# Optimization experiments

Hardware: AMD Instinct MI355X
Metric: run time of the kernel (lower is better)

## Reference

```python
import jax, jax.numpy as jnp
import numpy as np
from jax import lax


def _conv(x, w):
    # x: [B,H,W,C], w: [kh,kw,Cin,Cout], stride 1, 'same' padding
    return lax.conv_general_dilated(x, w, window_strides=(1, 1), padding='SAME',
                                    dimension_numbers=('NHWC', 'HWIO', 'NHWC'))


def setup_inputs() -> dict:
    key = jax.random.key(0)
    ks = jax.random.split(key, 4)
    B, T, H, W, Cin, F = 16, 5, 256, 256, 3, 8
    return {
        'input_tensor': jax.random.normal(ks[0], (B, T, H, W, Cin), jnp.float32),
        'kernel': jax.random.normal(ks[1], (3, 3, Cin, 4 * F), jnp.float32) * 0.1,
        'recurrent_kernel': jax.random.normal(ks[2], (3, 3, F, 4 * F), jnp.float32) * 0.1,
        'bias': jnp.zeros((4 * F,), jnp.float32),
        'gamma': jnp.ones((F,), jnp.float32),
        'beta': jnp.zeros((F,), jnp.float32),
        'moving_mean': jnp.zeros((F,), jnp.float32),
        'moving_var': jnp.ones((F,), jnp.float32),
        'dense_w': jax.random.normal(ks[3], (F, 2), jnp.float32) * 0.1,
        'dense_b': jnp.zeros((2,), jnp.float32),
    }


def reference(input_tensor, kernel, recurrent_kernel, bias, gamma, beta,
              moving_mean, moving_var, dense_w, dense_b):
    B, T, H, W, Cin = input_tensor.shape
    F = recurrent_kernel.shape[2]
    xs = jnp.moveaxis(input_tensor, 1, 0)  # [T,B,H,W,Cin] time-major for scan
    h0 = jnp.zeros((B, H, W, F), input_tensor.dtype)

    def step(carry, x_t):
        h, c = carry
        # fused 4-gate pre-activations, Keras gate order: i, f, c(g), o
        z = _conv(x_t, kernel) + _conv(h, recurrent_kernel) + bias
        i, f, g, o = jnp.split(z, 4, axis=-1)
        i = jax.nn.sigmoid(i)
        f = jax.nn.sigmoid(f)
        g = jnp.tanh(g)
        o = jax.nn.sigmoid(o)
        c = f * c + i * g
        h = o * jnp.tanh(c)
        return (h, c), None

    (h, _), _ = lax.scan(step, (h0, h0), xs)  # return_sequences=False -> last h

    # BatchNormalization (inference, Keras eps=1e-3)
    eps = 1e-3
    x = (h - moving_mean) * lax.rsqrt(moving_var + eps) * gamma + beta
    # LeakyReLU, Keras default alpha=0.3
    x = jnp.where(x >= 0, x, 0.3 * x)
    # Dense(2) over channel dim
    return jnp.einsum('bhwf,fk->bhwk', x, dense_w) + dense_b
```

## Files before the change

kernel.cpp:

```cpp
#include <hip/hip_runtime.h>


#define BB  16
#define TT  5
#define HH  256
#define WW  256
#define CIN 3
#define FF  8
#define GG  32

#define TW  32
#define THT 16
#define LW  34
#define LH  18
#define NG  8

#define SW  30
#define SH  14
#define NPX 9
#define NPY 19
#define NTILE (NPX * NPY * BB)
#define NBLKP 912

#define LOG2E 1.44269504088896340736f

typedef _Float16 half8  __attribute__((ext_vector_type(8)));
typedef _Float16 half4  __attribute__((ext_vector_type(4)));
typedef _Float16 half2t __attribute__((ext_vector_type(2)));
typedef float    floatx4 __attribute__((ext_vector_type(4)));

__device__ __forceinline__ float frcp(float x) { return __builtin_amdgcn_rcpf(x); }
__device__ __forceinline__ float sig2(float z)  { return frcp(1.0f + __builtin_amdgcn_exp2f(z)); }
__device__ __forceinline__ float tanh2(float z) { return 1.0f - 2.0f * frcp(1.0f + __builtin_amdgcn_exp2f(z)); }

__device__ __forceinline__ int clampi(int v, int lo, int hi) {
    return v < lo ? lo : (v > hi ? hi : v);
}

#define MFMA(A, B, C) __builtin_amdgcn_mfma_f32_16x16x32_f16((A), (B), (C), 0, 0, 0)

#define GATES(ACC0, ACC1, C0, C1, CN0, CN1, HN0, HN1)                         \
  float CN0, CN1, HN0, HN1;                                                   \
  {                                                                           \
    float s0 = lo8 ? ACC0[2] : ACC0[0]; float r0 = __shfl_xor(s0, 8, 64);     \
    float s1 = lo8 ? ACC0[3] : ACC0[1]; float r1 = __shfl_xor(s1, 8, 64);     \
    float s2 = lo8 ? ACC1[2] : ACC1[0]; float r2 = __shfl_xor(s2, 8, 64);     \
    float s3 = lo8 ? ACC1[3] : ACC1[1]; float r3 = __shfl_xor(s3, 8, 64);     \
    const float zi0 = lo8 ? ACC0[0] : r0, zi1 = lo8 ? ACC0[1] : r1;           \
    const float zf0 = lo8 ? r0 : ACC0[2], zf1 = lo8 ? r1 : ACC0[3];           \
    const float zg0 = lo8 ? ACC1[0] : r2, zg1 = lo8 ? ACC1[1] : r3;           \
    const float zo0 = lo8 ? r2 : ACC1[2], zo1 = lo8 ? r3 : ACC1[3];           \
    const float ii0 = sig2(zi0), ff0 = sig2(zf0), gg0 = tanh2(zg0), oo0 = sig2(zo0); \
    CN0 = ff0 * (C0) + ii0 * gg0;                                             \
    HN0 = oo0 * tanh2(CN0 * (2.0f * LOG2E));                                  \
    const float ii1 = sig2(zi1), ff1 = sig2(zf1), gg1 = tanh2(zg1), oo1 = sig2(zo1); \
    CN1 = ff1 * (C1) + ii1 * gg1;                                             \
    HN1 = oo1 * tanh2(CN1 * (2.0f * LOG2E));                                  \
  }

__global__ void build_frags(const float* __restrict__ wk,
                            const float* __restrict__ wr,
                            _Float16* __restrict__ blob) {
    const int lane = threadIdx.x & 63;
    const int quad = lane >> 4, nlo = lane & 15;
    for (int chunk = 0; chunk < 5; ++chunk) {
        for (int nh = 0; nh < 2; ++nh) {
            const int n = nh * 16 + nlo;
            const float scale = (n >= 16 && n < 24) ? (2.0f * LOG2E) : (-LOG2E);
            const int frag = chunk * 2 + nh;
            _Float16* dhi = blob + ((size_t)frag * 64 + lane) * 8;
            _Float16* dlo = (chunk >= 2)
                ? blob + ((size_t)(10 + (chunk - 2) * 2 + nh) * 64 + lane) * 8
                : nullptr;
            for (int j = 0; j < 8; ++j) {
                const int k = quad * 8 + j;
                float w = 0.0f;
                if (chunk == 0) {
                    int tap = k >> 2, ci = k & 3;
                    if (ci < 3) w = wk[(tap * 3 + ci) * GG + n];
                } else if (chunk == 1) {
                    if (quad == 0 && j < 3) w = wk[(8 * 3 + j) * GG + n];
                } else {
                    int c = chunk - 2;
                    int tap = c * 4 + quad, ci = j;
                    if (tap < 9) w = wr[(tap * FF + ci) * GG + n];
                }
                w *= scale;
                _Float16 wh = (_Float16)w;
                dhi[j] = wh;
                if (dlo) dlo[j] = (_Float16)(w - (float)wh);
            }
        }
    }
}

template <int FIRSTPAIR>
__global__ __launch_bounds__(256) void lstm_pair(
    const float* __restrict__ xg,
    int t,
    const _Float16* __restrict__ blob,
    const float* __restrict__ bias,
    const _Float16* __restrict__ hin,
    _Float16* __restrict__ hout,
    const _Float16* __restrict__ cin,
    _Float16* __restrict__ cout)
{
    __shared__ half8 hls1[LH * LW];
    __shared__ half4 xls1[LH * LW];
    __shared__ half4 xls2[THT * TW];
    __shared__ __align__(16) _Float16 hls2[THT * TW * FF];

    const int tid  = threadIdx.x;
    const int lane = tid & 63, wave = tid >> 6;
    const int quad = lane >> 4, nlo = lane & 15;
    const bool lo8 = (nlo < 8);
    const int fc = nlo & 7;
    const int m0 = quad * 4 + (lo8 ? 0 : 2);

    half8 bfh[10], bfl[6];
#pragma unroll
    for (int i = 0; i < 10; ++i)
        bfh[i] = *(const half8*)(blob + ((size_t)i * 64 + lane) * 8);
#pragma unroll
    for (int i = 0; i < 6; ++i)
        bfl[i] = *(const half8*)(blob + ((size_t)(10 + i) * 64 + lane) * 8);

    const float bv0 = bias[nlo] * (-LOG2E);
    const float bv1 = bias[16 + nlo] * (lo8 ? 2.0f * LOG2E : -LOG2E);

#pragma unroll 1
    for (int tile = (int)blockIdx.x; tile < NTILE; tile += NBLKP) {
        const int b  = tile / (NPX * NPY);
        const int rm = tile - b * (NPX * NPY);
        const int by = rm / NPX;
        const int bx = rm - by * NPX;
        const int x0 = bx * SW - 1, y0 = by * SH - 1;

        float xr1[3][3];
        bool  xin1[3];
#pragma unroll
        for (int k = 0; k < 3; ++k) {
            const int l = tid + k * 256;
            const bool in = (l < LH * LW);
            xin1[k] = in;
            int r = l / LW, c = l - r * LW;
            int gy = y0 - 1 + r, gx = x0 - 1 + c;
            const bool inb = in && (unsigned)gy < HH && (unsigned)gx < WW;
            const float* p = xg + (((size_t)(b * TT + t) * HH + gy) * WW + gx) * CIN;
            xr1[k][0] = inb ? p[0] : 0.0f;
            xr1[k][1] = inb ? p[1] : 0.0f;
            xr1[k][2] = inb ? p[2] : 0.0f;
        }
        float xr2[2][3];
#pragma unroll
        for (int k = 0; k < 2; ++k) {
            const int l = tid + k * 256;
            int r = l >> 5, c = l & 31;
            int gy = y0 + r, gx = x0 + c;
            const bool inb = (unsigned)gy < HH && (unsigned)gx < WW;
            const float* p = xg + (((size_t)(b * TT + t + 1) * HH + gy) * WW + gx) * CIN;
            xr2[k][0] = inb ? p[0] : 0.0f;
            xr2[k][1] = inb ? p[1] : 0.0f;
            xr2[k][2] = inb ? p[2] : 0.0f;
        }
        half8 hr[3];
        if (!FIRSTPAIR) {
#pragma unroll
            for (int k = 0; k < 3; ++k) {
                const int l = tid + k * 256;
                const bool in = (l < LH * LW);
                int r = l / LW, c = l - r * LW;
                int gy = y0 - 1 + r, gx = x0 - 1 + c;
                const bool inb = in && (unsigned)gy < HH && (unsigned)gx < WW;
                half8 v = {(_Float16)0, (_Float16)0, (_Float16)0, (_Float16)0,
                           (_Float16)0, (_Float16)0, (_Float16)0, (_Float16)0};
                if (inb) v = *(const half8*)(hin + ((size_t)(b * HH + gy) * WW + gx) * FF);
                hr[k] = v;
            }
        }
        half2t cpre[NG];
        if (!FIRSTPAIR) {
#pragma unroll
            for (int g = 0; g < NG; ++g) {
                const int lr  = wave * 4 + (g >> 1);
                const int gx0 = (g & 1) * 16;
                const int gy  = y0 + lr;
                const int gxa = x0 + gx0 + m0;
                const bool iny = (unsigned)gy < HH;
                half2t cv; cv.x = (_Float16)0; cv.y = (_Float16)0;
                const _Float16* cp = cin + ((size_t)(b * HH + gy) * WW + gxa) * FF + fc;
                if (iny && (unsigned)gxa < WW)       cv.x = cp[0];
                if (iny && (unsigned)(gxa + 1) < WW) cv.y = cp[FF];
                cpre[g] = cv;
            }
        }

        __syncthreads();

#pragma unroll
        for (int k = 0; k < 3; ++k) {
            if (xin1[k]) {
                half4 vh;
                vh.x = (_Float16)xr1[k][0];
                vh.y = (_Float16)xr1[k][1];
                vh.z = (_Float16)xr1[k][2];
                vh.w = (_Float16)0;
                xls1[tid + k * 256] = vh;
            }
        }
#pragma unroll
        for (int k = 0; k < 2; ++k) {
            half4 vh;
            vh.x = (_Float16)xr2[k][0];
            vh.y = (_Float16)xr2[k][1];
            vh.z = (_Float16)xr2[k][2];
            vh.w = (_Float16)0;
            xls2[tid + k * 256] = vh;
        }
        if (!FIRSTPAIR) {
#pragma unroll
            for (int k = 0; k < 3; ++k)
                if (xin1[k]) hls1[tid + k * 256] = hr[k];
        }
        __syncthreads();

        half2t creg[NG];
#pragma unroll
        for (int g = 0; g < NG; ++g) {
            const int lr  = wave * 4 + (g >> 1);
            const int gx0 = (g & 1) * 16;
            const int lc  = gx0 + nlo;

            const int t0 = 2 * quad, t1 = t0 + 1;
            half4 p  = xls1[(lr + t0 / 3) * LW + lc + t0 % 3];
            half4 q  = xls1[(lr + t1 / 3) * LW + lc + t1 % 3];
            half4 s8 = xls1[(lr + 2) * LW + lc + 2];
            half8 a_xA = (half8){p.x, p.y, p.z, p.w, q.x, q.y, q.z, q.w};
            half8 a_xB = (half8){s8.x, s8.y, s8.z, s8.w, s8.x, s8.y, s8.z, s8.w};

            floatx4 acc0 = {bv0, bv0, bv0, bv0};
            floatx4 acc1 = {bv1, bv1, bv1, bv1};
            acc0 = MFMA(a_xA, bfh[0], acc0);  acc1 = MFMA(a_xA, bfh[1], acc1);
            acc0 = MFMA(a_xB, bfh[2], acc0);  acc1 = MFMA(a_xB, bfh[3], acc1);
            if (!FIRSTPAIR) {
#pragma unroll
                for (int c = 0; c < 3; ++c) {
                    int tap = c * 4 + quad;
                    if (tap > 8) tap = 8;
                    half8 ah = hls1[(lr + tap / 3) * LW + lc + tap % 3];
                    acc0 = MFMA(ah, bfh[4 + c * 2], acc0);
                    acc1 = MFMA(ah, bfh[5 + c * 2], acc1);
                    acc0 = MFMA(ah, bfl[c * 2 + 0], acc0);
                    acc1 = MFMA(ah, bfl[c * 2 + 1], acc1);
                }
            }

            GATES(acc0, acc1,
                  FIRSTPAIR ? 0.0f : (float)cpre[g].x,
                  FIRSTPAIR ? 0.0f : (float)cpre[g].y,
                  cn0, cn1, hn0, hn1);

            half2t cc; cc.x = (_Float16)cn0; cc.y = (_Float16)cn1;
            creg[g] = cc;

            const int gy   = y0 + lr;
            const int colm = gx0 + m0;
            const int gxa  = x0 + colm;
            const bool iny = (unsigned)gy < HH;
            _Float16 h0v = (_Float16)hn0, h1v = (_Float16)hn1;
            if (!(iny && (unsigned)gxa < WW))       h0v = (_Float16)0;
            if (!(iny && (unsigned)(gxa + 1) < WW)) h1v = (_Float16)0;
            hls2[(lr * TW + colm) * FF + fc]     = h0v;
            hls2[(lr * TW + colm + 1) * FF + fc] = h1v;
        }
        __syncthreads();

#pragma unroll
        for (int g = 0; g < NG; ++g) {
            const int lr  = wave * 4 + (g >> 1);
            const int gx0 = (g & 1) * 16;
            const int lc  = gx0 + nlo;

            const int t0 = 2 * quad, t1 = t0 + 1;
            half4 p  = xls2[clampi(lr + t0 / 3 - 1, 0, THT - 1) * TW + clampi(lc + t0 % 3 - 1, 0, TW - 1)];
            half4 q  = xls2[clampi(lr + t1 / 3 - 1, 0, THT - 1) * TW + clampi(lc + t1 % 3 - 1, 0, TW - 1)];
            half4 s8 = xls2[clampi(lr + 1, 0, THT - 1) * TW + clampi(lc + 1, 0, TW - 1)];
            half8 a_xA = (half8){p.x, p.y, p.z, p.w, q.x, q.y, q.z, q.w};
            half8 a_xB = (half8){s8.x, s8.y, s8.z, s8.w, s8.x, s8.y, s8.z, s8.w};

            floatx4 acc0 = {bv0, bv0, bv0, bv0};
            floatx4 acc1 = {bv1, bv1, bv1, bv1};
            acc0 = MFMA(a_xA, bfh[0], acc0);  acc1 = MFMA(a_xA, bfh[1], acc1);
            acc0 = MFMA(a_xB, bfh[2], acc0);  acc1 = MFMA(a_xB, bfh[3], acc1);
#pragma unroll
            for (int c = 0; c < 3; ++c) {
                int tap = c * 4 + quad;
                if (tap > 8) tap = 8;
                const int rr = clampi(lr + tap / 3 - 1, 0, THT - 1);
                const int cc = clampi(lc + tap % 3 - 1, 0, TW - 1);
                half8 ah = *(const half8*)(hls2 + (rr * TW + cc) * FF);
                acc0 = MFMA(ah, bfh[4 + c * 2], acc0);
                acc1 = MFMA(ah, bfh[5 + c * 2], acc1);
                acc0 = MFMA(ah, bfl[c * 2 + 0], acc0);
                acc1 = MFMA(ah, bfl[c * 2 + 1], acc1);
            }

            GATES(acc0, acc1, (float)creg[g].x, (float)creg[g].y, cn0, cn1, hn0, hn1);

            const int gy   = y0 + lr;
            const int colm = gx0 + m0;
            const int gxa  = x0 + colm;
            const bool rowok = (lr >= 1) && (lr <= SH) && ((unsigned)gy < HH);
            const bool c0ok = rowok && (colm >= 1) && (colm <= SW) && ((unsigned)gxa < WW);
            const bool c1ok = rowok && (colm + 1 <= SW) && ((unsigned)(gxa + 1) < WW);
            const size_t base = ((size_t)(b * HH + gy) * WW + gxa) * FF + fc;
            if (c0ok) {
                hout[base] = (_Float16)hn0;
                cout[base] = (_Float16)cn0;
            }
            if (c1ok) {
                hout[base + FF] = (_Float16)hn1;
                cout[base + FF] = (_Float16)cn1;
            }
        }
    }
}

__global__ __launch_bounds__(256) void lstm_last(
    const float* __restrict__ xg,
    const _Float16* __restrict__ blob,
    const float* __restrict__ bias,
    const _Float16* __restrict__ hin,
    const _Float16* __restrict__ cin,
    const float* __restrict__ gamma, const float* __restrict__ beta,
    const float* __restrict__ mean,  const float* __restrict__ var,
    const float* __restrict__ dw,    const float* __restrict__ db,
    float* __restrict__ out)
{
    __shared__ half8 hls[LH * LW];
    __shared__ half4 xls[LH * LW];

    const int tid  = threadIdx.x;
    const int lane = tid & 63, wave = tid >> 6;
    const int quad = lane >> 4, nlo = lane & 15;
    const bool lo8 = (nlo < 8);
    const int fc = nlo & 7;
    const int m0 = quad * 4 + (lo8 ? 0 : 2);
    const int bx = blockIdx.x, by = blockIdx.y, b = blockIdx.z;
    const int t = TT - 1;

    half8 bfh[10], bfl[6];
#pragma unroll
    for (int i = 0; i < 10; ++i)
        bfh[i] = *(const half8*)(blob + ((size_t)i * 64 + lane) * 8);
#pragma unroll
    for (int i = 0; i < 6; ++i)
        bfl[i] = *(const half8*)(blob + ((size_t)(10 + i) * 64 + lane) * 8);

    const float bv0 = bias[nlo] * (-LOG2E);
    const float bv1 = bias[16 + nlo] * (lo8 ? 2.0f * LOG2E : -LOG2E);

    float xr[3][3];
    bool  xin[3];
#pragma unroll
    for (int k = 0; k < 3; ++k) {
        const int l = tid + k * 256;
        const bool in = (l < LH * LW);
        xin[k] = in;
        int r = l / LW, c = l - r * LW;
        int gy = by * THT + r - 1, gx = bx * TW + c - 1;
        const bool inb = in && (unsigned)gy < HH && (unsigned)gx < WW;
        const float* p = xg + (((size_t)(b * TT + t) * HH + gy) * WW + gx) * CIN;
        xr[k][0] = inb ? p[0] : 0.0f;
        xr[k][1] = inb ? p[1] : 0.0f;
        xr[k][2] = inb ? p[2] : 0.0f;
    }
    half8 hr[3];
#pragma unroll
    for (int k = 0; k < 3; ++k) {
        const int l = tid + k * 256;
        const bool in = (l < LH * LW);
        int r = l / LW, c = l - r * LW;
        int gy = by * THT + r - 1, gx = bx * TW + c - 1;
        const bool inb = in && (unsigned)gy < HH && (unsigned)gx < WW;
        half8 v = {(_Float16)0, (_Float16)0, (_Float16)0, (_Float16)0,
                   (_Float16)0, (_Float16)0, (_Float16)0, (_Float16)0};
        if (inb) v = *(const half8*)(hin + ((size_t)(b * HH + gy) * WW + gx) * FF);
        hr[k] = v;
    }
    half2t cpre[NG];
#pragma unroll
    for (int g = 0; g < NG; ++g) {
        const int lr  = wave * 4 + (g >> 1);
        const int gx0 = (g & 1) * 16;
        const int gy  = by * THT + lr;
        const int gxa = bx * TW + gx0 + m0;
        const _Float16* cp = cin + ((size_t)(b * HH + gy) * WW + gxa) * FF + fc;
        half2t cv; cv.x = cp[0]; cv.y = cp[FF];
        cpre[g] = cv;
    }

#pragma unroll
    for (int k = 0; k < 3; ++k) {
        if (xin[k]) {
            half4 vh;
            vh.x = (_Float16)xr[k][0];
            vh.y = (_Float16)xr[k][1];
            vh.z = (_Float16)xr[k][2];
            vh.w = (_Float16)0;
            xls[tid + k * 256] = vh;
            hls[tid + k * 256] = hr[k];
        }
    }
    __syncthreads();

    const float bn_s = gamma[fc] * rsqrtf(var[fc] + 1e-3f);
    const float bn_b = beta[fc] - mean[fc] * bn_s;
    const float dw0 = dw[fc * 2 + 0], dw1 = dw[fc * 2 + 1];
    const float db0 = db[0], db1 = db[1];

#pragma unroll
    for (int g = 0; g < NG; ++g) {
        const int lr  = wave * 4 + (g >> 1);
        const int gx0 = (g & 1) * 16;
        const int lc  = gx0 + nlo;

        const int t0 = 2 * quad, t1 = t0 + 1;
        half4 p  = xls[(lr + t0 / 3) * LW + lc + t0 % 3];
        half4 q  = xls[(lr + t1 / 3) * LW + lc + t1 % 3];
        half4 s8 = xls[(lr + 2) * LW + lc + 2];
        half8 a_xA = (half8){p.x, p.y, p.z, p.w, q.x, q.y, q.z, q.w};
        half8 a_xB = (half8){s8.x, s8.y, s8.z, s8.w, s8.x, s8.y, s8.z, s8.w};

        floatx4 acc0 = {bv0, bv0, bv0, bv0};
        floatx4 acc1 = {bv1, bv1, bv1, bv1};
        acc0 = MFMA(a_xA, bfh[0], acc0);  acc1 = MFMA(a_xA, bfh[1], acc1);
        acc0 = MFMA(a_xB, bfh[2], acc0);  acc1 = MFMA(a_xB, bfh[3], acc1);
#pragma unroll
        for (int c = 0; c < 3; ++c) {
            int tap = c * 4 + quad;
            if (tap > 8) tap = 8;
            half8 ah = hls[(lr + tap / 3) * LW + lc + tap % 3];
            acc0 = MFMA(ah, bfh[4 + c * 2], acc0);
            acc1 = MFMA(ah, bfh[5 + c * 2], acc1);
            acc0 = MFMA(ah, bfl[c * 2 + 0], acc0);
            acc1 = MFMA(ah, bfl[c * 2 + 1], acc1);
        }

        GATES(acc0, acc1, (float)cpre[g].x, (float)cpre[g].y, cn0, cn1, hn0, hn1);
        (void)cn0; (void)cn1;

        const int gy = by * THT + lr;
        float y0 = bn_s * hn0 + bn_b; y0 = (y0 >= 0.f) ? y0 : 0.3f * y0;
        float y1 = bn_s * hn1 + bn_b; y1 = (y1 >= 0.f) ? y1 : 0.3f * y1;
        float p00 = y0 * dw0, p01 = y0 * dw1;
        float p10 = y1 * dw0, p11 = y1 * dw1;
#pragma unroll
        for (int m = 1; m <= 4; m <<= 1) {
            p00 += __shfl_xor(p00, m, 64);
            p01 += __shfl_xor(p01, m, 64);
            p10 += __shfl_xor(p10, m, 64);
            p11 += __shfl_xor(p11, m, 64);
        }
        const int j = nlo & 7;
        if (j < 4) {
            const int px = m0 + (j >> 1);
            const int k  = j & 1;
            float val = (j == 0 ? p00 : j == 1 ? p01 : j == 2 ? p10 : p11)
                        + (k ? db1 : db0);
            out[((size_t)(b * HH + gy) * WW + bx * TW + gx0 + px) * 2 + k] = val;
        }
    }
}

extern "C" void kernel_launch(void* const* d_in, const int* in_sizes, int n_in,
                              void* d_out, int out_size, void* d_ws, size_t ws_size,
                              hipStream_t stream) {
    const float* x     = (const float*)d_in[0];
    const float* wk    = (const float*)d_in[1];
    const float* wr    = (const float*)d_in[2];
    const float* bias  = (const float*)d_in[3];
    const float* gamma = (const float*)d_in[4];
    const float* beta  = (const float*)d_in[5];
    const float* mean  = (const float*)d_in[6];
    const float* var   = (const float*)d_in[7];
    const float* dw    = (const float*)d_in[8];
    const float* db    = (const float*)d_in[9];
    float* out = (float*)d_out;

    const size_t state = (size_t)BB * HH * WW * FF;
    _Float16* blob = (_Float16*)d_ws;
    _Float16* hA = (_Float16*)((char*)d_ws + 32768);
    _Float16* hB = hA + state;
    _Float16* cA = hB + state;
    _Float16* cB = cA + state;

    build_frags<<<1, 64, 0, stream>>>(wk, wr, blob);

    dim3 block(256);
    lstm_pair<1><<<dim3(NBLKP), block, 0, stream>>>(x, 0, blob, bias,
                                                    nullptr, hA, nullptr, cA);
    lstm_pair<0><<<dim3(NBLKP), block, 0, stream>>>(x, 2, blob, bias,
                                                    hA, hB, cA, cB);
    dim3 lgrid(WW / TW, HH / THT, BB);
    lstm_last<<<lgrid, block, 0, stream>>>(x, blob, bias, hB, cB,
                                           gamma, beta, mean, var, dw, db, out);
}
```

Before: 298.4 us.

## Cut register pressure: move low-half weights to LDS, defer halo loads, raise occupancy

```diff
diff --git a/kernel.cpp b/kernel.cpp
--- a/kernel.cpp
+++ b/kernel.cpp
@@ -95,7 +95,7 @@
 }
 
 template <int FIRSTPAIR>
-__global__ __launch_bounds__(256) void lstm_pair(
+__global__ __launch_bounds__(256, 3) void lstm_pair(
     const float* __restrict__ xg,
     int t,
     const _Float16* __restrict__ blob,
@@ -109,6 +109,7 @@
     __shared__ half4 xls1[LH * LW];
     __shared__ half4 xls2[THT * TW];
     __shared__ __align__(16) _Float16 hls2[THT * TW * FF];
+    __shared__ half8 bflds[6 * 64];
 
     const int tid  = threadIdx.x;
     const int lane = tid & 63, wave = tid >> 6;
@@ -117,13 +118,13 @@
     const int fc = nlo & 7;
     const int m0 = quad * 4 + (lo8 ? 0 : 2);
 
-    half8 bfh[10], bfl[6];
+    for (int i = tid; i < 6 * 64; i += 256)
+        bflds[i] = *(const half8*)(blob + ((size_t)(10 + (i >> 6)) * 64 + (i & 63)) * 8);
+
+    half8 bfh[10];
 #pragma unroll
     for (int i = 0; i < 10; ++i)
         bfh[i] = *(const half8*)(blob + ((size_t)i * 64 + lane) * 8);
-#pragma unroll
-    for (int i = 0; i < 6; ++i)
-        bfl[i] = *(const half8*)(blob + ((size_t)(10 + i) * 64 + lane) * 8);
 
     const float bv0 = bias[nlo] * (-LOG2E);
     const float bv1 = bias[16 + nlo] * (lo8 ? 2.0f * LOG2E : -LOG2E);
@@ -136,48 +137,6 @@
         const int bx = rm - by * NPX;
         const int x0 = bx * SW - 1, y0 = by * SH - 1;
 
-        float xr1[3][3];
-        bool  xin1[3];
-#pragma unroll
-        for (int k = 0; k < 3; ++k) {
-            const int l = tid + k * 256;
-            const bool in = (l < LH * LW);
-            xin1[k] = in;
-            int r = l / LW, c = l - r * LW;
-            int gy = y0 - 1 + r, gx = x0 - 1 + c;
-            const bool inb = in && (unsigned)gy < HH && (unsigned)gx < WW;
-            const float* p = xg + (((size_t)(b * TT + t) * HH + gy) * WW + gx) * CIN;
-            xr1[k][0] = inb ? p[0] : 0.0f;
-            xr1[k][1] = inb ? p[1] : 0.0f;
-            xr1[k][2] = inb ? p[2] : 0.0f;
-        }
-        float xr2[2][3];
-#pragma unroll
-        for (int k = 0; k < 2; ++k) {
-            const int l = tid + k * 256;
-            int r = l >> 5, c = l & 31;
-            int gy = y0 + r, gx = x0 + c;
-            const bool inb = (unsigned)gy < HH && (unsigned)gx < WW;
-            const float* p = xg + (((size_t)(b * TT + t + 1) * HH + gy) * WW + gx) * CIN;
-            xr2[k][0] = inb ? p[0] : 0.0f;
-            xr2[k][1] = inb ? p[1] : 0.0f;
-            xr2[k][2] = inb ? p[2] : 0.0f;
-        }
-        half8 hr[3];
-        if (!FIRSTPAIR) {
-#pragma unroll
-            for (int k = 0; k < 3; ++k) {
-                const int l = tid + k * 256;
-                const bool in = (l < LH * LW);
-                int r = l / LW, c = l - r * LW;
-                int gy = y0 - 1 + r, gx = x0 - 1 + c;
-                const bool inb = in && (unsigned)gy < HH && (unsigned)gx < WW;
-                half8 v = {(_Float16)0, (_Float16)0, (_Float16)0, (_Float16)0,
-                           (_Float16)0, (_Float16)0, (_Float16)0, (_Float16)0};
-                if (inb) v = *(const half8*)(hin + ((size_t)(b * HH + gy) * WW + gx) * FF);
-                hr[k] = v;
-            }
-        }
         half2t cpre[NG];
         if (!FIRSTPAIR) {
 #pragma unroll
@@ -194,18 +153,51 @@
                 cpre[g] = cv;
             }
         }
+        float xr2[2][3];
+#pragma unroll
+        for (int k = 0; k < 2; ++k) {
+            const int l = tid + k * 256;
+            int r = l >> 5, c = l & 31;
+            int gy = y0 + r, gx = x0 + c;
+            const bool inb = (unsigned)gy < HH && (unsigned)gx < WW;
+            const float* p = xg + (((size_t)(b * TT + t + 1) * HH + gy) * WW + gx) * CIN;
+            xr2[k][0] = inb ? p[0] : 0.0f;
+            xr2[k][1] = inb ? p[1] : 0.0f;
+            xr2[k][2] = inb ? p[2] : 0.0f;
+        }
 
         __syncthreads();
 
 #pragma unroll
         for (int k = 0; k < 3; ++k) {
-            if (xin1[k]) {
+            const int l = tid + k * 256;
+            if (l < LH * LW) {
+                int r = l / LW, c = l - r * LW;
+                int gy = y0 - 1 + r, gx = x0 - 1 + c;
+                const bool inb = (unsigned)gy < HH && (unsigned)gx < WW;
+                const float* p = xg + (((size_t)(b * TT + t) * HH + gy) * WW + gx) * CIN;
+                float v0 = inb ? p[0] : 0.0f;
+                float v1 = inb ? p[1] : 0.0f;
+                float v2 = inb ? p[2] : 0.0f;
                 half4 vh;
-                vh.x = (_Float16)xr1[k][0];
-                vh.y = (_Float16)xr1[k][1];
-                vh.z = (_Float16)xr1[k][2];
-                vh.w = (_Float16)0;
-                xls1[tid + k * 256] = vh;
+                vh.x = (_Float16)v0; vh.y = (_Float16)v1;
+                vh.z = (_Float16)v2; vh.w = (_Float16)0;
+                xls1[l] = vh;
+            }
+        }
+        if (!FIRSTPAIR) {
+#pragma unroll
+            for (int k = 0; k < 3; ++k) {
+                const int l = tid + k * 256;
+                if (l < LH * LW) {
+                    int r = l / LW, c = l - r * LW;
+                    int gy = y0 - 1 + r, gx = x0 - 1 + c;
+                    const bool inb = (unsigned)gy < HH && (unsigned)gx < WW;
+                    half8 v = {(_Float16)0, (_Float16)0, (_Float16)0, (_Float16)0,
+                               (_Float16)0, (_Float16)0, (_Float16)0, (_Float16)0};
+                    if (inb) v = *(const half8*)(hin + ((size_t)(b * HH + gy) * WW + gx) * FF);
+                    hls1[l] = v;
+                }
             }
         }
 #pragma unroll
@@ -217,11 +209,6 @@
             vh.w = (_Float16)0;
             xls2[tid + k * 256] = vh;
         }
-        if (!FIRSTPAIR) {
-#pragma unroll
-            for (int k = 0; k < 3; ++k)
-                if (xin1[k]) hls1[tid + k * 256] = hr[k];
-        }
         __syncthreads();
 
         half2t creg[NG];
@@ -250,8 +237,8 @@
                     half8 ah = hls1[(lr + tap / 3) * LW + lc + tap % 3];
                     acc0 = MFMA(ah, bfh[4 + c * 2], acc0);
                     acc1 = MFMA(ah, bfh[5 + c * 2], acc1);
-                    acc0 = MFMA(ah, bfl[c * 2 + 0], acc0);
-                    acc1 = MFMA(ah, bfl[c * 2 + 1], acc1);
+                    acc0 = MFMA(ah, bflds[(c * 2 + 0) * 64 + lane], acc0);
+                    acc1 = MFMA(ah, bflds[(c * 2 + 1) * 64 + lane], acc1);
                 }
             }
 
@@ -301,8 +288,8 @@
                 half8 ah = *(const half8*)(hls2 + (rr * TW + cc) * FF);
                 acc0 = MFMA(ah, bfh[4 + c * 2], acc0);
                 acc1 = MFMA(ah, bfh[5 + c * 2], acc1);
-                acc0 = MFMA(ah, bfl[c * 2 + 0], acc0);
-                acc1 = MFMA(ah, bfl[c * 2 + 1], acc1);
+                acc0 = MFMA(ah, bflds[(c * 2 + 0) * 64 + lane], acc0);
+                acc1 = MFMA(ah, bflds[(c * 2 + 1) * 64 + lane], acc1);
             }
 
             GATES(acc0, acc1, (float)creg[g].x, (float)creg[g].y, cn0, cn1, hn0, hn1);
@@ -326,7 +313,7 @@
     }
 }
 
-__global__ __launch_bounds__(256) void lstm_last(
+__global__ __launch_bounds__(256, 3) void lstm_last(
     const float* __restrict__ xg,
     const _Float16* __restrict__ blob,
     const float* __restrict__ bias,
@@ -339,6 +326,7 @@
 {
     __shared__ half8 hls[LH * LW];
     __shared__ half4 xls[LH * LW];
+    __shared__ half8 bflds[6 * 64];
 
     const int tid  = threadIdx.x;
     const int lane = tid & 63, wave = tid >> 6;
@@ -349,45 +337,17 @@
     const int bx = blockIdx.x, by = blockIdx.y, b = blockIdx.z;
     const int t = TT - 1;
 
-    half8 bfh[10], bfl[6];
+    for (int i = tid; i < 6 * 64; i += 256)
+        bflds[i] = *(const half8*)(blob + ((size_t)(10 + (i >> 6)) * 64 + (i & 63)) * 8);
+
+    half8 bfh[10];
 #pragma unroll
     for (int i = 0; i < 10; ++i)
         bfh[i] = *(const half8*)(blob + ((size_t)i * 64 + lane) * 8);
-#pragma unroll
-    for (int i = 0; i < 6; ++i)
-        bfl[i] = *(const half8*)(blob + ((size_t)(10 + i) * 64 + lane) * 8);
 
     const float bv0 = bias[nlo] * (-LOG2E);
     const float bv1 = bias[16 + nlo] * (lo8 ? 2.0f * LOG2E : -LOG2E);
 
-    float xr[3][3];
-    bool  xin[3];
-#pragma unroll
-    for (int k = 0; k < 3; ++k) {
-        const int l = tid + k * 256;
-        const bool in = (l < LH * LW);
-        xin[k] = in;
-        int r = l / LW, c = l - r * LW;
-        int gy = by * THT + r - 1, gx = bx * TW + c - 1;
-        const bool inb = in && (unsigned)gy < HH && (unsigned)gx < WW;
-        const float* p = xg + (((size_t)(b * TT + t) * HH + gy) * WW + gx) * CIN;
-        xr[k][0] = inb ? p[0] : 0.0f;
-        xr[k][1] = inb ? p[1] : 0.0f;
-        xr[k][2] = inb ? p[2] : 0.0f;
-    }
-    half8 hr[3];
-#pragma unroll
-    for (int k = 0; k < 3; ++k) {
-        const int l = tid + k * 256;
-        const bool in = (l < LH * LW);
-        int r = l / LW, c = l - r * LW;
-        int gy = by * THT + r - 1, gx = bx * TW + c - 1;
-        const bool inb = in && (unsigned)gy < HH && (unsigned)gx < WW;
-        half8 v = {(_Float16)0, (_Float16)0, (_Float16)0, (_Float16)0,
-                   (_Float16)0, (_Float16)0, (_Float16)0, (_Float16)0};
-        if (inb) v = *(const half8*)(hin + ((size_t)(b * HH + gy) * WW + gx) * FF);
-        hr[k] = v;
-    }
     half2t cpre[NG];
 #pragma unroll
     for (int g = 0; g < NG; ++g) {
@@ -402,14 +362,23 @@
 
 #pragma unroll
     for (int k = 0; k < 3; ++k) {
-        if (xin[k]) {
+        const int l = tid + k * 256;
+        if (l < LH * LW) {
+            int r = l / LW, c = l - r * LW;
+            int gy = by * THT + r - 1, gx = bx * TW + c - 1;
+            const bool inb = (unsigned)gy < HH && (unsigned)gx < WW;
+            const float* p = xg + (((size_t)(b * TT + t) * HH + gy) * WW + gx) * CIN;
+            float v0 = inb ? p[0] : 0.0f;
+            float v1 = inb ? p[1] : 0.0f;
+            float v2 = inb ? p[2] : 0.0f;
             half4 vh;
-            vh.x = (_Float16)xr[k][0];
-            vh.y = (_Float16)xr[k][1];
-            vh.z = (_Float16)xr[k][2];
-            vh.w = (_Float16)0;
-            xls[tid + k * 256] = vh;
-            hls[tid + k * 256] = hr[k];
+            vh.x = (_Float16)v0; vh.y = (_Float16)v1;
+            vh.z = (_Float16)v2; vh.w = (_Float16)0;
+            xls[l] = vh;
+            half8 v = {(_Float16)0, (_Float16)0, (_Float16)0, (_Float16)0,
+                       (_Float16)0, (_Float16)0, (_Float16)0, (_Float16)0};
+            if (inb) v = *(const half8*)(hin + ((size_t)(b * HH + gy) * WW + gx) * FF);
+            hls[l] = v;
         }
     }
     __syncthreads();
@@ -443,8 +412,8 @@
             half8 ah = hls[(lr + tap / 3) * LW + lc + tap % 3];
             acc0 = MFMA(ah, bfh[4 + c * 2], acc0);
             acc1 = MFMA(ah, bfh[5 + c * 2], acc1);
-            acc0 = MFMA(ah, bfl[c * 2 + 0], acc0);
-            acc1 = MFMA(ah, bfl[c * 2 + 1], acc1);
+            acc0 = MFMA(ah, bflds[(c * 2 + 0) * 64 + lane], acc0);
+            acc1 = MFMA(ah, bflds[(c * 2 + 1) * 64 + lane], acc1);
         }
 
         GATES(acc0, acc1, (float)cpre[g].x, (float)cpre[g].y, cn0, cn1, hn0, hn1);
```

New measurement: 404.4 us. 1.36x slower.
